# Optimization experiments

Measured on AMD Instinct MI355X. Metric: run time of the kernel, lower is better.

## Reference

```python
import jax, jax.numpy as jnp
import numpy as np

N_NODES = 100000
IN_CH = 512
OUT_CH = 64
N_EDGES = 1600000
NEG_SLOPE = 0.2  # PyG GATv2Conv default negative_slope


def setup_inputs() -> dict:
    key = jax.random.key(0)
    ks = jax.random.split(key, 8)
    x = jax.random.normal(ks[0], (N_NODES, IN_CH), dtype=jnp.float32)
    edge_index = jax.random.randint(ks[1], (2, N_EDGES), 0, N_NODES, dtype=jnp.int64)
    s_in = 1.0 / np.sqrt(IN_CH)
    s_out = 1.0 / np.sqrt(OUT_CH)
    W_l = jax.random.uniform(ks[2], (IN_CH, OUT_CH), jnp.float32, -s_in, s_in)
    b_l = jnp.zeros((OUT_CH,), jnp.float32)
    W_r = jax.random.uniform(ks[3], (IN_CH, OUT_CH), jnp.float32, -s_in, s_in)
    b_r = jnp.zeros((OUT_CH,), jnp.float32)
    att = jax.random.uniform(ks[4], (OUT_CH,), jnp.float32, -s_out, s_out)
    bias = jnp.zeros((OUT_CH,), jnp.float32)
    return {"x": x, "edge_index": edge_index, "W_l": W_l, "b_l": b_l,
            "W_r": W_r, "b_r": b_r, "att": att, "bias": bias}


def reference(x, edge_index, W_l, b_l, W_r, b_r, att, bias):
    n = x.shape[0]
    # add self loops (PyG GATv2Conv default add_self_loops=True)
    loop = jnp.arange(n, dtype=edge_index.dtype)
    src = jnp.concatenate([edge_index[0], loop])  # source j
    dst = jnp.concatenate([edge_index[1], loop])  # target i

    x_l = x @ W_l + b_l  # [N, D] source-side transform
    x_r = x @ W_r + b_r  # [N, D] target-side transform

    # GATv2 attention logit per edge: att . LeakyReLU(x_l[j] + x_r[i])
    z = x_l[src] + x_r[dst]                       # [E, D]
    z = jnp.where(z > 0, z, NEG_SLOPE * z)
    logits = z @ att                               # [E]

    # segment softmax over incoming edges of each target node
    seg_max = jax.ops.segment_max(logits, dst, num_segments=n)
    seg_max = jnp.where(jnp.isfinite(seg_max), seg_max, 0.0)
    e = jnp.exp(logits - seg_max[dst])
    denom = jax.ops.segment_sum(e, dst, num_segments=n)
    alpha = e / jnp.maximum(denom[dst], 1e-16)     # [E]

    # weighted scatter-add aggregation of source features
    out = jax.ops.segment_sum(alpha[:, None] * x_l[src], dst, num_segments=n)
    return out + bias
```

## Files before the change

kernel.cpp:

```cpp
#include <hip/hip_runtime.h>
#include <hip/hip_bf16.h>

constexpr int IC = 512;
constexpr int OC = 64;
#define NEG_SLOPE 0.2f

constexpr int EPB = 4096;
constexpr int NBK = 128;
constexpr int BKSHIFT = 10;
constexpr int BKSIZE = 1024;

typedef __attribute__((ext_vector_type(8))) __bf16 bf16x8;
typedef __attribute__((ext_vector_type(4))) float f32x4;
typedef unsigned short u16;

__device__ __forceinline__ float bf2f(u16 h) {
  return __uint_as_float(((unsigned)h) << 16);
}

__global__ __launch_bounds__(256)
void k_shuffleB(const float* __restrict__ Wl, const float* __restrict__ Wr,
                __hip_bfloat16* __restrict__ Bp) {
  const int tid = blockIdx.x * 256 + threadIdx.x;
  if (tid >= 8 * 16 * 64) return;
  const int lane = tid & 63;
  const int kb = (tid >> 6) & 15;
  const int cb = tid >> 10;
  const int col = cb * 16 + (lane & 15);
  const int k0 = kb * 32 + (lane >> 4) * 8;
  const float* W = (col < OC) ? (Wl + col) : (Wr + (col - OC));
  bf16x8 v;
  #pragma unroll
  for (int j = 0; j < 8; ++j) v[j] = (__bf16)W[(size_t)(k0 + j) * OC];
  *(bf16x8*)(Bp + (size_t)tid * 8) = v;
}

__device__ inline bf16x8 cvt8(const float4& a, const float4& b) {
  bf16x8 r;
  r[0] = (__bf16)a.x; r[1] = (__bf16)a.y; r[2] = (__bf16)a.z; r[3] = (__bf16)a.w;
  r[4] = (__bf16)b.x; r[5] = (__bf16)b.y; r[6] = (__bf16)b.z; r[7] = (__bf16)b.w;
  return r;
}

__device__ __forceinline__ void gload_lds16(const float* g, const float* l) {
  __builtin_amdgcn_global_load_lds(
      (const __attribute__((address_space(1))) float*)(uintptr_t)g,
      (__attribute__((address_space(3))) float*)(uintptr_t)l,
      16, 0, 0);
}

__global__ __launch_bounds__(256)
void k_gemm(const float* __restrict__ x, const __hip_bfloat16* __restrict__ Bp,
            const float* __restrict__ bl, const float* __restrict__ br,
            __bf16* __restrict__ xl, __bf16* __restrict__ xr, int n) {
  __shared__ float As[2][128 * 32];
  const int t = threadIdx.x;
  const int lane = t & 63;
  const int w = t >> 6;
  const int l15 = lane & 15, lg = lane >> 4;
  const int rowbase_g = blockIdx.x * 128 + w * 32;

  const float* srcp[4];
  #pragma unroll
  for (int j = 0; j < 4; ++j) {
    const int row_l = w * 32 + j * 8 + (lane >> 3);
    const int grow = min(blockIdx.x * 128 + row_l, n - 1);
    const int gch = (lane & 7) ^ (row_l & 7);
    srcp[j] = x + (size_t)grow * IC + gch * 4;
  }
  const bf16x8* pb = (const bf16x8*)Bp + lane;

  f32x4 acc[2][8] = {};

  #pragma unroll
  for (int j = 0; j < 4; ++j)
    gload_lds16(srcp[j], &As[0][w * 1024 + j * 256]);

  int buf = 0;
  for (int kt = 0; kt < 16; ++kt) {
    bf16x8 bfr[8];
    #pragma unroll
    for (int cb = 0; cb < 8; ++cb)
      bfr[cb] = pb[(cb * 16 + kt) * 64];
    asm volatile("s_waitcnt vmcnt(8)" ::: "memory");
    if (kt < 15) {
      #pragma unroll
      for (int j = 0; j < 4; ++j)
        gload_lds16(srcp[j] + (kt + 1) * 32, &As[buf ^ 1][w * 1024 + j * 256]);
    }
    #pragma unroll
    for (int rg = 0; rg < 2; ++rg) {
      const int row = rg * 16 + l15;
      const int s0 = (2 * lg) ^ (row & 7);
      const int s1 = (2 * lg + 1) ^ (row & 7);
      const int rbase = (w * 32 + row) * 32;
      const float4 f0 = *(const float4*)&As[buf][rbase + s0 * 4];
      const float4 f1 = *(const float4*)&As[buf][rbase + s1 * 4];
      const bf16x8 af = cvt8(f0, f1);
      #pragma unroll
      for (int cb = 0; cb < 8; ++cb)
        acc[rg][cb] = __builtin_amdgcn_mfma_f32_16x16x32_bf16(af, bfr[cb], acc[rg][cb], 0, 0, 0);
    }
    buf ^= 1;
  }

  #pragma unroll
  for (int cb = 0; cb < 8; ++cb) {
    const int col = cb * 16 + l15;
    __bf16* dst = (col < OC) ? xl : xr;
    const int c2 = col & (OC - 1);
    const float bv = (col < OC) ? bl[c2] : br[c2];
    #pragma unroll
    for (int rg = 0; rg < 2; ++rg) {
      const int rb = rowbase_g + rg * 16 + lg * 4;
      #pragma unroll
      for (int q = 0; q < 4; ++q)
        if (rb + q < n) dst[(size_t)(rb + q) * OC + c2] = (__bf16)(acc[rg][cb][q] + bv);
    }
  }
}

__global__ __launch_bounds__(256)
void k_bin1a(const int* __restrict__ edst, int* __restrict__ slen,
             int E, int nch) {
  __shared__ int lcnt[NBK];
  const int t = threadIdx.x;
  const int c = blockIdx.x;
  const int e0 = c * EPB;
  if (t < NBK) lcnt[t] = 0;
  __syncthreads();
  #pragma unroll
  for (int j = 0; j < 16; ++j) {
    const int i = e0 + j * 256 + t;
    if (i < E) atomicAdd(&lcnt[edst[i] >> BKSHIFT], 1);
  }
  __syncthreads();
  if (t < NBK) slen[t * nch + c] = lcnt[t];
}

__global__ __launch_bounds__(256)
void k_colscan(int* __restrict__ slen, int* __restrict__ btot, int nch) {
  __shared__ int sm[256];
  const int t = threadIdx.x;
  const int base = blockIdx.x * nch;
  const int per = (nch + 255) / 256;
  int v[8];
  int s = 0;
  for (int k = 0; k < per; ++k) {
    const int idx = t * per + k;
    v[k] = (idx < nch) ? slen[base + idx] : 0;
    s += v[k];
  }
  sm[t] = s;
  __syncthreads();
  #pragma unroll
  for (int d = 1; d < 256; d <<= 1) {
    int u = (t >= d) ? sm[t - d] : 0;
    __syncthreads();
    sm[t] += u;
    __syncthreads();
  }
  int run = (t == 0) ? 0 : sm[t - 1];
  for (int k = 0; k < per; ++k) {
    const int idx = t * per + k;
    if (idx < nch) slen[base + idx] = run;
    run += v[k];
  }
  if (t == 255) btot[blockIdx.x] = sm[255];
}

__global__ __launch_bounds__(256)
void k_bscan(const int* __restrict__ btot, int* __restrict__ bbase, int nbk) {
  __shared__ int sm[256];
  const int t = threadIdx.x;
  const int v = (t < nbk) ? btot[t] : 0;
  sm[t] = v;
  __syncthreads();
  #pragma unroll
  for (int d = 1; d < 256; d <<= 1) {
    int u = (t >= d) ? sm[t - d] : 0;
    __syncthreads();
    sm[t] += u;
    __syncthreads();
  }
  if (t < NBK) bbase[t] = sm[t] - v;
  if (t == NBK - 1) bbase[NBK] = sm[t];
}

__global__ __launch_bounds__(256)
void k_bin1b(const int* __restrict__ esrc, const int* __restrict__ edst,
             const int* __restrict__ slen, const int* __restrict__ bbase,
             int* __restrict__ bstage, int E, int nch) {
  __shared__ int lcnt[NBK];
  __shared__ int lbase[NBK];
  __shared__ int ldst[NBK];
  __shared__ int lword[EPB];
  __shared__ unsigned char lbkt[EPB];
  __shared__ int sm[256];
  const int t = threadIdx.x;
  const int c = blockIdx.x;
  const int e0 = c * EPB;
  if (t < NBK) lcnt[t] = 0;
  __syncthreads();

  int s_[16], d_[16], r_[16];
  #pragma unroll
  for (int j = 0; j < 16; ++j) {
    const int i = e0 + j * 256 + t;
    if (i < E) {
      s_[j] = esrc[i];
      d_[j] = edst[i];
      r_[j] = atomicAdd(&lcnt[d_[j] >> BKSHIFT], 1);
    }
  }
  __syncthreads();
  const int vv = (t < NBK) ? lcnt[t] : 0;
  sm[t] = vv;
  __syncthreads();
  #pragma unroll
  for (int d = 1; d < 256; d <<= 1) {
    int u = (t >= d) ? sm[t - d] : 0;
    __syncthreads();
    sm[t] += u;
    __syncthreads();
  }
  if (t < NBK) {
    lbase[t] = sm[t] - vv;
    ldst[t] = bbase[t] + slen[t * nch + c];
  }
  __syncthreads();
  #pragma unroll
  for (int j = 0; j < 16; ++j) {
    const int i = e0 + j * 256 + t;
    if (i < E) {
      const int b = d_[j] >> BKSHIFT;
      const int pos = lbase[b] + r_[j];
      lword[pos] = (s_[j] << BKSHIFT) | (d_[j] & (BKSIZE - 1));
      lbkt[pos] = (unsigned char)b;
    }
  }
  __syncthreads();
  const int used = min(E - e0, EPB);
  for (int k = t; k < used; k += 256) {
    const int b = lbkt[k];
    bstage[ldst[b] + (k - lbase[b])] = lword[k];
  }
}

__global__ __launch_bounds__(1024)
void k_bcount(const int* __restrict__ bstage, const int* __restrict__ bbase,
              int* __restrict__ cnt, int n) {
  __shared__ int lc[BKSIZE];
  const int t = threadIdx.x;
  const int b = blockIdx.x;
  const int node0 = b << BKSHIFT;
  lc[t] = 0;
  __syncthreads();
  const int end = bbase[b + 1];
  for (int k = bbase[b] + t; k < end; k += 1024)
    atomicAdd(&lc[bstage[k] & (BKSIZE - 1)], 1);
  __syncthreads();
  if (node0 + t < n) cnt[node0 + t] = lc[t] + 1;
}

__global__ __launch_bounds__(256)
void k_scan1(const int* __restrict__ cnt, int* __restrict__ bsum, int n) {
  __shared__ int sm[4];
  const int t = threadIdx.x;
  const int base = blockIdx.x * 1024 + t * 4;
  int s = 0;
  #pragma unroll
  for (int j = 0; j < 4; ++j) {
    const int i = base + j;
    if (i < n) s += cnt[i];
  }
  #pragma unroll
  for (int d = 1; d < 64; d <<= 1) s += __shfl_xor(s, d);
  if ((t & 63) == 0) sm[t >> 6] = s;
  __syncthreads();
  if (t == 0) bsum[blockIdx.x] = sm[0] + sm[1] + sm[2] + sm[3];
}

__global__ __launch_bounds__(1024)
void k_scan2(int* __restrict__ bsum, int* __restrict__ off, int nb, int n) {
  __shared__ int sm[1024];
  const int t = threadIdx.x;
  sm[t] = (t < nb) ? bsum[t] : 0;
  __syncthreads();
  #pragma unroll
  for (int d = 1; d < 1024; d <<= 1) {
    int v = (t >= d) ? sm[t - d] : 0;
    __syncthreads();
    sm[t] += v;
    __syncthreads();
  }
  if (t < nb) bsum[t] = (t == 0) ? 0 : sm[t - 1];
  if (t == nb - 1) off[n] = sm[t];
}

__global__ __launch_bounds__(256)
void k_scan3(const int* __restrict__ cnt, const int* __restrict__ bsum,
             int* __restrict__ off, int n) {
  __shared__ int sm[256];
  const int t = threadIdx.x;
  const int base = blockIdx.x * 1024 + t * 4;
  int v[4];
  int s = 0;
  #pragma unroll
  for (int j = 0; j < 4; ++j) {
    const int i = base + j;
    v[j] = (i < n) ? cnt[i] : 0;
    s += v[j];
  }
  sm[t] = s;
  __syncthreads();
  #pragma unroll
  for (int d = 1; d < 256; d <<= 1) {
    int u = (t >= d) ? sm[t - d] : 0;
    __syncthreads();
    sm[t] += u;
    __syncthreads();
  }
  int run = bsum[blockIdx.x] + ((t == 0) ? 0 : sm[t - 1]);
  #pragma unroll
  for (int j = 0; j < 4; ++j) {
    const int i = base + j;
    if (i < n) off[i] = run;
    run += v[j];
  }
}

__global__ __launch_bounds__(1024)
void k_bplace(const int* __restrict__ bstage, const int* __restrict__ bbase,
              const int* __restrict__ off, int* __restrict__ rec, int n) {
  __shared__ int lcur[BKSIZE];
  const int t = threadIdx.x;
  const int b = blockIdx.x;
  const int node0 = b << BKSHIFT;
  if (node0 + t < n) {
    const int o = off[node0 + t];
    rec[o] = node0 + t;
    lcur[t] = o + 1;
  }
  __syncthreads();
  const int end = bbase[b + 1];
  for (int k = bbase[b] + t; k < end; k += 1024) {
    const int w = bstage[k];
    const int pos = atomicAdd(&lcur[w & (BKSIZE - 1)], 1);
    rec[pos] = w >> BKSHIFT;
  }
}

__global__ __launch_bounds__(256)
void k_gather(const int* __restrict__ off, const int* __restrict__ rec,
              const u16* __restrict__ xl, const u16* __restrict__ xr,
              const float* __restrict__ att, const float* __restrict__ bias,
              float* __restrict__ out, int n) {
  const int lane = threadIdx.x & 63;
  const int node = (blockIdx.x * 256 + threadIdx.x) >> 6;
  if (node >= n) return;
  const int slot = lane >> 4;
  const int c4 = (lane & 15) * 4;

  const ushort4 xrh = *(const ushort4*)(xr + (size_t)node * OC + c4);
  const float4 xrv = make_float4(bf2f(xrh.x), bf2f(xrh.y), bf2f(xrh.z), bf2f(xrh.w));
  const float4 aw  = *(const float4*)(att + c4);

  const int beg = off[node];
  const int end = off[node + 1];
  float denom = 0.0f;
  float4 acc = make_float4(0.f, 0.f, 0.f, 0.f);

  int p = beg + slot;
  bool cv = (p < end);
  ushort4 xh = make_ushort4(0, 0, 0, 0);
  if (cv) {
    const int s = rec[p];
    xh = *(const ushort4*)(xl + (size_t)s * OC + c4);
  }
  for (int base = beg; base < end; base += 4) {
    const ushort4 ch = xh;
    const bool curv = cv;
    p += 4;
    cv = (p < end);
    if (cv) {
      const int s = rec[p];
      xh = *(const ushort4*)(xl + (size_t)s * OC + c4);
    } else {
      xh = make_ushort4(0, 0, 0, 0);
    }
    const float4 cur = make_float4(bf2f(ch.x), bf2f(ch.y), bf2f(ch.z), bf2f(ch.w));
    float zx = cur.x + xrv.x; zx = zx > 0.f ? zx : NEG_SLOPE * zx;
    float zy = cur.y + xrv.y; zy = zy > 0.f ? zy : NEG_SLOPE * zy;
    float zz = cur.z + xrv.z; zz = zz > 0.f ? zz : NEG_SLOPE * zz;
    float zw = cur.w + xrv.w; zw = zw > 0.f ? zw : NEG_SLOPE * zw;
    float lg = zx * aw.x + zy * aw.y + zz * aw.z + zw * aw.w;
    lg += __shfl_xor(lg, 1);
    lg += __shfl_xor(lg, 2);
    lg += __shfl_xor(lg, 4);
    lg += __shfl_xor(lg, 8);
    const float wgt = curv ? __expf(lg) : 0.0f;
    denom += wgt;
    acc.x = fmaf(wgt, cur.x, acc.x);
    acc.y = fmaf(wgt, cur.y, acc.y);
    acc.z = fmaf(wgt, cur.z, acc.z);
    acc.w = fmaf(wgt, cur.w, acc.w);
  }
  denom += __shfl_xor(denom, 16);
  denom += __shfl_xor(denom, 32);
  acc.x += __shfl_xor(acc.x, 16); acc.x += __shfl_xor(acc.x, 32);
  acc.y += __shfl_xor(acc.y, 16); acc.y += __shfl_xor(acc.y, 32);
  acc.z += __shfl_xor(acc.z, 16); acc.z += __shfl_xor(acc.z, 32);
  acc.w += __shfl_xor(acc.w, 16); acc.w += __shfl_xor(acc.w, 32);

  if (slot == 0) {
    const float4 bv = *(const float4*)(bias + c4);
    const float inv = 1.0f / denom;
    float4 o;
    o.x = acc.x * inv + bv.x;
    o.y = acc.y * inv + bv.y;
    o.z = acc.z * inv + bv.z;
    o.w = acc.w * inv + bv.w;
    *(float4*)(out + (size_t)node * OC + c4) = o;
  }
}

extern "C" void kernel_launch(void* const* d_in, const int* in_sizes, int n_in,
                              void* d_out, int out_size, void* d_ws, size_t ws_size,
                              hipStream_t stream) {
  const float* x    = (const float*)d_in[0];
  const int*   ei   = (const int*)d_in[1];
  const float* Wl   = (const float*)d_in[2];
  const float* bl   = (const float*)d_in[3];
  const float* Wr   = (const float*)d_in[4];
  const float* br   = (const float*)d_in[5];
  const float* att  = (const float*)d_in[6];
  const float* bias = (const float*)d_in[7];
  float* out = (float*)d_out;

  const int n = in_sizes[0] / IC;
  const int E = in_sizes[1] / 2;
  const int total = E + n;
  const int* esrc = ei;
  const int* edst = ei + E;
  const int nb = (n + 1023) / 1024;
  const int nch = (E + EPB - 1) / EPB;
  const int nbk = (n + BKSIZE - 1) >> BKSHIFT;

  char* wp = (char*)d_ws;
  __hip_bfloat16* Bp = (__hip_bfloat16*)wp;  wp += 131072;
  __bf16* xl  = (__bf16*)wp;                 wp += (size_t)n * OC * 2;
  __bf16* xr  = (__bf16*)wp;                 wp += (size_t)n * OC * 2;
  int* bstage = (int*)wp;                    wp += (size_t)E * 4;
  int* slen   = (int*)wp;                    wp += (size_t)NBK * nch * 4;
  int* btot   = (int*)wp;                    wp += (size_t)NBK * 4;
  int* bbase  = (int*)wp;                    wp += (size_t)(NBK + 1) * 4;
  int* cnt    = (int*)wp;                    wp += (size_t)n * 4;
  int* off    = (int*)wp;                    wp += (size_t)(n + 1) * 4;
  int* bsum   = (int*)wp;                    wp += (size_t)nb * 4;
  int* rec    = (int*)wp;                    wp += (size_t)total * 4;

  k_shuffleB<<<32, 256, 0, stream>>>(Wl, Wr, Bp);
  k_gemm<<<(n + 127) / 128, 256, 0, stream>>>(x, Bp, bl, br, xl, xr, n);
  k_bin1a<<<nch, 256, 0, stream>>>(edst, slen, E, nch);
  k_colscan<<<nbk, 256, 0, stream>>>(slen, btot, nch);
  k_bscan<<<1, 256, 0, stream>>>(btot, bbase, nbk);
  k_bin1b<<<nch, 256, 0, stream>>>(esrc, edst, slen, bbase, bstage, E, nch);
  k_bcount<<<nbk, 1024, 0, stream>>>(bstage, bbase, cnt, n);
  k_scan1<<<nb, 256, 0, stream>>>(cnt, bsum, n);
  k_scan2<<<1, 1024, 0, stream>>>(bsum, off, nb, n);
  k_scan3<<<nb, 256, 0, stream>>>(cnt, bsum, off, n);
  k_bplace<<<nbk, 1024, 0, stream>>>(bstage, bbase, off, rec, n);
  k_gather<<<((size_t)n * 64 + 255) / 256, 256, 0, stream>>>(off, rec, (const u16*)xl, (const u16*)xr, att, bias, out, n);
}
```

Before: 191.5 us.

## Triple-buffer A tiles and double-buffer B fragments in the projection GEMM

Deepens the k_gemm software pipeline: A tiles are prefetched two k-steps ahead into a three-slot LDS ring, and B fragments are loaded one step ahead into alternating register sets. The vmcnt waits are adjusted to match. The aim is to hide global memory latency in the x projection. It costs more LDS per block (48KB), which may reduce occupancy, and more registers.

Result: no change. 188.7 us (-1.4%).

```diff
diff --git a/kernel.cpp b/kernel.cpp
--- a/kernel.cpp
+++ b/kernel.cpp
@@ -53,7 +53,7 @@
 void k_gemm(const float* __restrict__ x, const __hip_bfloat16* __restrict__ Bp,
             const float* __restrict__ bl, const float* __restrict__ br,
             __bf16* __restrict__ xl, __bf16* __restrict__ xr, int n) {
-  __shared__ float As[2][128 * 32];
+  __shared__ float As[3][128 * 32];
   const int t = threadIdx.x;
   const int lane = t & 63;
   const int w = t >> 6;
@@ -71,37 +71,52 @@
   const bf16x8* pb = (const bf16x8*)Bp + lane;
 
   f32x4 acc[2][8] = {};
+  bf16x8 bA[8], bB[8];
 
   #pragma unroll
   for (int j = 0; j < 4; ++j)
     gload_lds16(srcp[j], &As[0][w * 1024 + j * 256]);
-
-  int buf = 0;
+  #pragma unroll
+  for (int cb = 0; cb < 8; ++cb) bA[cb] = pb[(cb * 16) * 64];
+  #pragma unroll
+  for (int j = 0; j < 4; ++j)
+    gload_lds16(srcp[j] + 32, &As[1][w * 1024 + j * 256]);
+
+  #pragma unroll
   for (int kt = 0; kt < 16; ++kt) {
-    bf16x8 bfr[8];
-    #pragma unroll
-    for (int cb = 0; cb < 8; ++cb)
-      bfr[cb] = pb[(cb * 16 + kt) * 64];
-    asm volatile("s_waitcnt vmcnt(8)" ::: "memory");
     if (kt < 15) {
+      if ((kt & 1) == 0) {
+        #pragma unroll
+        for (int cb = 0; cb < 8; ++cb) bB[cb] = pb[(cb * 16 + kt + 1) * 64];
+      } else {
+        #pragma unroll
+        for (int cb = 0; cb < 8; ++cb) bA[cb] = pb[(cb * 16 + kt + 1) * 64];
+      }
+    }
+    if (kt <= 13) {
+      const int nb3 = (kt + 2) % 3;
       #pragma unroll
       for (int j = 0; j < 4; ++j)
-        gload_lds16(srcp[j] + (kt + 1) * 32, &As[buf ^ 1][w * 1024 + j * 256]);
-    }
+        gload_lds16(srcp[j] + (kt + 2) * 32, &As[nb3][w * 1024 + j * 256]);
+    }
+    if (kt <= 13)      asm volatile("s_waitcnt vmcnt(16)" ::: "memory");
+    else if (kt == 14) asm volatile("s_waitcnt vmcnt(12)" ::: "memory");
+    else               asm volatile("s_waitcnt vmcnt(0)" ::: "memory");
+    const int cb3 = kt % 3;
     #pragma unroll
     for (int rg = 0; rg < 2; ++rg) {
       const int row = rg * 16 + l15;
       const int s0 = (2 * lg) ^ (row & 7);
       const int s1 = (2 * lg + 1) ^ (row & 7);
       const int rbase = (w * 32 + row) * 32;
-      const float4 f0 = *(const float4*)&As[buf][rbase + s0 * 4];
-      const float4 f1 = *(const float4*)&As[buf][rbase + s1 * 4];
+      const float4 f0 = *(const float4*)&As[cb3][rbase + s0 * 4];
+      const float4 f1 = *(const float4*)&As[cb3][rbase + s1 * 4];
       const bf16x8 af = cvt8(f0, f1);
       #pragma unroll
       for (int cb = 0; cb < 8; ++cb)
-        acc[rg][cb] = __builtin_amdgcn_mfma_f32_16x16x32_bf16(af, bfr[cb], acc[rg][cb], 0, 0, 0);
-    }
-    buf ^= 1;
+        acc[rg][cb] = __builtin_amdgcn_mfma_f32_16x16x32_bf16(
+            af, ((kt & 1) == 0) ? bA[cb] : bB[cb], acc[rg][cb], 0, 0, 0);
+    }
   }
 
   #pragma unroll
```

## Double K-tile depth in GEMM with explicit asm loads and scheduling barriers

Applied to the files above, without the earlier changes.

The projection GEMM now stages 64-wide K tiles (8 iterations instead of 16) in a larger double-buffered LDS array with a 16-chunk XOR swizzle. B fragment loads and LDS reads move to inline asm, with explicit waitcnts and sched_barriers, and the loop is fully unrolled. The goal is fewer loop iterations and barriers, and better overlap of global prefetch with MFMA work. In exchange, LDS use doubles to 64KB per block, which may lower occupancy, and register pressure rises from 16 B fragments plus 8 float4 values.

Result: faster. 185.3 us (-3.2%).

```diff
diff --git a/kernel.cpp b/kernel.cpp
--- a/kernel.cpp
+++ b/kernel.cpp
@@ -13,6 +13,7 @@
 typedef __attribute__((ext_vector_type(8))) __bf16 bf16x8;
 typedef __attribute__((ext_vector_type(4))) float f32x4;
 typedef unsigned short u16;
+typedef unsigned int u32;
 
 __device__ __forceinline__ float bf2f(u16 h) {
   return __uint_as_float(((unsigned)h) << 16);
@@ -49,59 +50,89 @@
       16, 0, 0);
 }
 
+__device__ __forceinline__ bf16x8 gload_b16(const void* p) {
+  bf16x8 r;
+  asm volatile("global_load_dwordx4 %0, %1, off" : "=v"(r) : "v"(p));
+  return r;
+}
+
+__device__ __forceinline__ float4 ds_read128(u32 a) {
+  float4 r;
+  asm volatile("ds_read_b128 %0, %1" : "=v"(r) : "v"(a));
+  return r;
+}
+
 __global__ __launch_bounds__(256)
 void k_gemm(const float* __restrict__ x, const __hip_bfloat16* __restrict__ Bp,
             const float* __restrict__ bl, const float* __restrict__ br,
             __bf16* __restrict__ xl, __bf16* __restrict__ xr, int n) {
-  __shared__ float As[2][128 * 32];
+  __shared__ float As[2][128 * 64];
   const int t = threadIdx.x;
   const int lane = t & 63;
   const int w = t >> 6;
   const int l15 = lane & 15, lg = lane >> 4;
   const int rowbase_g = blockIdx.x * 128 + w * 32;
 
-  const float* srcp[4];
-  #pragma unroll
-  for (int j = 0; j < 4; ++j) {
-    const int row_l = w * 32 + j * 8 + (lane >> 3);
+  const float* srcp[8];
+  #pragma unroll
+  for (int j = 0; j < 8; ++j) {
+    const int row_l = w * 32 + j * 4 + lg;
     const int grow = min(blockIdx.x * 128 + row_l, n - 1);
-    const int gch = (lane & 7) ^ (row_l & 7);
+    const int gch = l15 ^ ((j * 4 + lg) & 15);
     srcp[j] = x + (size_t)grow * IC + gch * 4;
   }
   const bf16x8* pb = (const bf16x8*)Bp + lane;
+  const u32 lds0 = (u32)(uintptr_t)&As[0][0];
+  const u32 lds1 = (u32)(uintptr_t)&As[1][0];
 
   f32x4 acc[2][8] = {};
 
   #pragma unroll
-  for (int j = 0; j < 4; ++j)
-    gload_lds16(srcp[j], &As[0][w * 1024 + j * 256]);
-
-  int buf = 0;
-  for (int kt = 0; kt < 16; ++kt) {
-    bf16x8 bfr[8];
+  for (int j = 0; j < 8; ++j)
+    gload_lds16(srcp[j], &As[0][w * 2048 + j * 256]);
+
+  #pragma unroll
+  for (int kt = 0; kt < 8; ++kt) {
+    bf16x8 bfr[16];
     #pragma unroll
-    for (int cb = 0; cb < 8; ++cb)
-      bfr[cb] = pb[(cb * 16 + kt) * 64];
-    asm volatile("s_waitcnt vmcnt(8)" ::: "memory");
-    if (kt < 15) {
-      #pragma unroll
-      for (int j = 0; j < 4; ++j)
-        gload_lds16(srcp[j] + (kt + 1) * 32, &As[buf ^ 1][w * 1024 + j * 256]);
-    }
-    #pragma unroll
-    for (int rg = 0; rg < 2; ++rg) {
-      const int row = rg * 16 + l15;
-      const int s0 = (2 * lg) ^ (row & 7);
-      const int s1 = (2 * lg + 1) ^ (row & 7);
-      const int rbase = (w * 32 + row) * 32;
-      const float4 f0 = *(const float4*)&As[buf][rbase + s0 * 4];
-      const float4 f1 = *(const float4*)&As[buf][rbase + s1 * 4];
-      const bf16x8 af = cvt8(f0, f1);
+    for (int kb = 0; kb < 2; ++kb)
       #pragma unroll
       for (int cb = 0; cb < 8; ++cb)
-        acc[rg][cb] = __builtin_amdgcn_mfma_f32_16x16x32_bf16(af, bfr[cb], acc[rg][cb], 0, 0, 0);
+        bfr[kb * 8 + cb] = gload_b16(pb + (cb * 16 + kt * 2 + kb) * 64);
+    __builtin_amdgcn_sched_barrier(0);
+    if (kt < 7) {
+      #pragma unroll
+      for (int j = 0; j < 8; ++j)
+        gload_lds16(srcp[j] + (kt + 1) * 64, &As[(kt + 1) & 1][w * 2048 + j * 256]);
     }
-    buf ^= 1;
+    __builtin_amdgcn_sched_barrier(0);
+    if (kt < 7) asm volatile("s_waitcnt vmcnt(8)" ::: "memory");
+    else        asm volatile("s_waitcnt vmcnt(0)" ::: "memory");
+    __builtin_amdgcn_sched_barrier(0);
+    const u32 lb = (kt & 1) ? lds1 : lds0;
+    float4 f[8];
+    #pragma unroll
+    for (int kb = 0; kb < 2; ++kb) {
+      const int kc0 = kb * 8 + lg * 2;
+      #pragma unroll
+      for (int rg = 0; rg < 2; ++rg) {
+        const int rbase = (w * 32 + rg * 16 + l15) * 64;
+        f[kb * 4 + rg * 2 + 0] = ds_read128(lb + (u32)(rbase + ((kc0 ^ l15) * 4)) * 4u);
+        f[kb * 4 + rg * 2 + 1] = ds_read128(lb + (u32)(rbase + (((kc0 + 1) ^ l15) * 4)) * 4u);
+      }
+    }
+    asm volatile("s_waitcnt lgkmcnt(0)" ::: "memory");
+    __builtin_amdgcn_sched_barrier(0);
+    #pragma unroll
+    for (int kb = 0; kb < 2; ++kb)
+      #pragma unroll
+      for (int rg = 0; rg < 2; ++rg) {
+        const bf16x8 af = cvt8(f[kb * 4 + rg * 2], f[kb * 4 + rg * 2 + 1]);
+        #pragma unroll
+        for (int cb = 0; cb < 8; ++cb)
+          acc[rg][cb] = __builtin_amdgcn_mfma_f32_16x16x32_bf16(
+              af, bfr[kb * 8 + cb], acc[rg][cb], 0, 0, 0);
+      }
   }
 
   #pragma unroll
```

## Retile GEMM to 64-row blocks with 64-wide K slabs

Applied to the files above, without the earlier changes.

Changes the projection GEMM block tile from 128 rows by 32 K to 64 rows by 64 K, with each wave owning 16 rows and the XOR swizzle widened to 16 chunks. The grid doubles so more blocks are in flight, and the K loop has half as many iterations, each loading two B fragments per column block. The aim is better occupancy and latency hiding on a memory-bound x read. In exchange, B fragments are reloaded per 64 rows instead of per 128, adding weight traffic, and per-thread register use for B fragments rises.

Result: no change. 191.6 us (+0.1%).

```diff
diff --git a/kernel.cpp b/kernel.cpp
--- a/kernel.cpp
+++ b/kernel.cpp
@@ -53,53 +53,53 @@
 void k_gemm(const float* __restrict__ x, const __hip_bfloat16* __restrict__ Bp,
             const float* __restrict__ bl, const float* __restrict__ br,
             __bf16* __restrict__ xl, __bf16* __restrict__ xr, int n) {
-  __shared__ float As[2][128 * 32];
+  __shared__ float As[2][64 * 64];
   const int t = threadIdx.x;
   const int lane = t & 63;
   const int w = t >> 6;
   const int l15 = lane & 15, lg = lane >> 4;
-  const int rowbase_g = blockIdx.x * 128 + w * 32;
+  const int rowbase_g = blockIdx.x * 64 + w * 16;
 
   const float* srcp[4];
   #pragma unroll
   for (int j = 0; j < 4; ++j) {
-    const int row_l = w * 32 + j * 8 + (lane >> 3);
-    const int grow = min(blockIdx.x * 128 + row_l, n - 1);
-    const int gch = (lane & 7) ^ (row_l & 7);
+    const int row_l = w * 16 + j * 4 + lg;
+    const int grow = min(blockIdx.x * 64 + row_l, n - 1);
+    const int gch = l15 ^ ((j * 4 + lg) & 15);
     srcp[j] = x + (size_t)grow * IC + gch * 4;
   }
   const bf16x8* pb = (const bf16x8*)Bp + lane;
 
-  f32x4 acc[2][8] = {};
+  f32x4 acc[8] = {};
 
   #pragma unroll
   for (int j = 0; j < 4; ++j)
     gload_lds16(srcp[j], &As[0][w * 1024 + j * 256]);
 
   int buf = 0;
-  for (int kt = 0; kt < 16; ++kt) {
-    bf16x8 bfr[8];
+  for (int kt = 0; kt < 8; ++kt) {
+    bf16x8 b0[8], b1[8];
     #pragma unroll
-    for (int cb = 0; cb < 8; ++cb)
-      bfr[cb] = pb[(cb * 16 + kt) * 64];
-    asm volatile("s_waitcnt vmcnt(8)" ::: "memory");
-    if (kt < 15) {
+    for (int cb = 0; cb < 8; ++cb) b0[cb] = pb[(cb * 16 + kt * 2 + 0) * 64];
+    #pragma unroll
+    for (int cb = 0; cb < 8; ++cb) b1[cb] = pb[(cb * 16 + kt * 2 + 1) * 64];
+    asm volatile("s_waitcnt vmcnt(16)" ::: "memory");
+    if (kt < 7) {
       #pragma unroll
       for (int j = 0; j < 4; ++j)
-        gload_lds16(srcp[j] + (kt + 1) * 32, &As[buf ^ 1][w * 1024 + j * 256]);
+        gload_lds16(srcp[j] + (kt + 1) * 64, &As[buf ^ 1][w * 1024 + j * 256]);
     }
+    const int rbase = (w * 16 + l15) * 64;
     #pragma unroll
-    for (int rg = 0; rg < 2; ++rg) {
-      const int row = rg * 16 + l15;
-      const int s0 = (2 * lg) ^ (row & 7);
-      const int s1 = (2 * lg + 1) ^ (row & 7);
-      const int rbase = (w * 32 + row) * 32;
-      const float4 f0 = *(const float4*)&As[buf][rbase + s0 * 4];
-      const float4 f1 = *(const float4*)&As[buf][rbase + s1 * 4];
+    for (int kb = 0; kb < 2; ++kb) {
+      const int kc0 = kb * 8 + lg * 2;
+      const float4 f0 = *(const float4*)&As[buf][rbase + ((kc0 ^ l15) * 4)];
+      const float4 f1 = *(const float4*)&As[buf][rbase + (((kc0 + 1) ^ l15) * 4)];
       const bf16x8 af = cvt8(f0, f1);
       #pragma unroll
       for (int cb = 0; cb < 8; ++cb)
-        acc[rg][cb] = __builtin_amdgcn_mfma_f32_16x16x32_bf16(af, bfr[cb], acc[rg][cb], 0, 0, 0);
+        acc[cb] = __builtin_amdgcn_mfma_f32_16x16x32_bf16(
+            af, (kb == 0) ? b0[cb] : b1[cb], acc[cb], 0, 0, 0);
     }
     buf ^= 1;
   }
@@ -110,13 +110,10 @@
     __bf16* dst = (col < OC) ? xl : xr;
     const int c2 = col & (OC - 1);
     const float bv = (col < OC) ? bl[c2] : br[c2];
+    const int rb = rowbase_g + lg * 4;
     #pragma unroll
-    for (int rg = 0; rg < 2; ++rg) {
-      const int rb = rowbase_g + rg * 16 + lg * 4;
-      #pragma unroll
-      for (int q = 0; q < 4; ++q)
-        if (rb + q < n) dst[(size_t)(rb + q) * OC + c2] = (__bf16)(acc[rg][cb][q] + bv);
-    }
+    for (int q = 0; q < 4; ++q)
+      if (rb + q < n) dst[(size_t)(rb + q) * OC + c2] = (__bf16)(acc[cb][q] + bv);
   }
 }
 
@@ -461,7 +458,7 @@
   int* rec    = (int*)wp;                    wp += (size_t)total * 4;
 
   k_shuffleB<<<32, 256, 0, stream>>>(Wl, Wr, Bp);
-  k_gemm<<<(n + 127) / 128, 256, 0, stream>>>(x, Bp, bl, br, xl, xr, n);
+  k_gemm<<<(n + 63) / 64, 256, 0, stream>>>(x, Bp, bl, br, xl, xr, n);
   k_bin1a<<<nch, 256, 0, stream>>>(edst, slen, E, nch);
   k_colscan<<<nbk, 256, 0, stream>>>(slen, btot, nch);
   k_bscan<<<1, 256, 0, stream>>>(btot, bbase, nbk);
```
